# Optimization experiments

Hardware: AMD Instinct MI355X
Metric: run time of the kernel (lower is better)

The kernel has to match this reference:

```python
import jax, jax.numpy as jnp
import numpy as np

B_, N_, E_, NNZ = 64, 1723, 1723, 16384
CIN, COUT = 256, 256
H1, H2, H3 = 64, 32, 128  # lin1 out, HGCN hidden, HGCN out (hidden_channels=128)


def layernorm(x, g, b, eps=1e-5):
    mu = jnp.mean(x, axis=-1, keepdims=True)
    var = jnp.mean((x - mu) ** 2, axis=-1, keepdims=True)
    return (x - mu) * jax.lax.rsqrt(var + eps) * g + b


def graph_linear(x, W, b):
    # x: (B, Cin, N) -> (B, Cout, N), matches torch.matmul(W[None], x) + b[None,:,None]
    return jnp.einsum('oc,bcn->bon', W, x) + b[None, :, None]


def hconv(x, node_idx, edge_idx, theta, bias):
    # PyG HypergraphConv (no attention): X' = D^-1 H W B^-1 H^T X Theta + bias
    x = jnp.einsum('bnc,oc->bno', x, theta)  # lin (bias=False)
    ones = jnp.ones(node_idx.shape, x.dtype)
    Dd = jax.ops.segment_sum(ones, node_idx, num_segments=N_)  # node degree
    Bd = jax.ops.segment_sum(ones, edge_idx, num_segments=E_)  # hyperedge degree
    Dinv = jnp.where(Dd > 0, 1.0 / Dd, 0.0)
    Binv = jnp.where(Bd > 0, 1.0 / Bd, 0.0)
    # node -> hyperedge aggregation, message scaled by B^-1 of target edge
    msg = jnp.swapaxes(x[:, node_idx, :] * Binv[edge_idx][None, :, None], 0, 1)  # (nnz,B,C)
    ef = jax.ops.segment_sum(msg, edge_idx, num_segments=E_)  # (E,B,C)
    # hyperedge -> node aggregation, message scaled by D^-1 of target node
    msg2 = ef[edge_idx] * Dinv[node_idx][:, None, None]  # (nnz,B,C)
    out = jax.ops.segment_sum(msg2, node_idx, num_segments=N_)  # (N,B,C)
    return jnp.swapaxes(out, 0, 1) + bias


def setup_inputs():
    key = jax.random.key(0)
    ks = jax.random.split(key, 8)
    s = 0.02
    return {
        'x': jax.random.normal(ks[0], (B_, N_, CIN), jnp.float32),
        'incident_matrix': jax.random.randint(ks[1], (2, NNZ), 0, N_, jnp.int32),
        'pre_g': jnp.ones((CIN,), jnp.float32),
        'pre_b': jnp.zeros((CIN,), jnp.float32),
        'lin1_W': jax.random.normal(ks[2], (H1, CIN), jnp.float32) * s,
        'lin1_b': jnp.zeros((H1,), jnp.float32),
        'n1_g': jnp.ones((H1,), jnp.float32),
        'n1_b': jnp.zeros((H1,), jnp.float32),
        'th1': jax.random.normal(ks[3], (H2, H1), jnp.float32) * s,
        'bi1': jnp.zeros((H2,), jnp.float32),
        'th2': jax.random.normal(ks[4], (H3, H2), jnp.float32) * s,
        'bi2': jnp.zeros((H3,), jnp.float32),
        'n2_g': jnp.ones((H3,), jnp.float32),
        'n2_b': jnp.zeros((H3,), jnp.float32),
        'lin2_W': jax.random.normal(ks[5], (COUT, H3), jnp.float32) * s,
        'lin2_b': jnp.zeros((COUT,), jnp.float32),
    }


def reference(x, incident_matrix, pre_g, pre_b, lin1_W, lin1_b, n1_g, n1_b,
              th1, bi1, th2, bi2, n2_g, n2_b, lin2_W, lin2_b):
    node_idx, edge_idx = incident_matrix[0], incident_matrix[1]
    ty = jnp.swapaxes(jax.nn.relu(layernorm(x, pre_g, pre_b)), 1, 2)  # (B,Cin,N)
    y = jnp.swapaxes(graph_linear(ty, lin1_W, lin1_b), 1, 2)          # (B,N,64)
    y = jax.nn.relu(layernorm(y, n1_g, n1_b))
    y = hconv(y, node_idx, edge_idx, th1, bi1)                         # (B,N,32)
    y = hconv(y, node_idx, edge_idx, th2, bi2)                         # (B,N,128)
    ty = jnp.swapaxes(jax.nn.relu(layernorm(y, n2_g, n2_b)), 1, 2)
    y = jnp.swapaxes(graph_linear(ty, lin2_W, lin2_b), 1, 2)           # (B,N,256)
    return x + y  # skip_conv declared in module but unused in forward
```

## Files before the change

### kernel.cpp

```cpp
#include <hip/hip_runtime.h>
#include <cstdint>

constexpr int B  = 64;
constexpr int N  = 1723;
constexpr int E  = 1723;
constexpr int NNZ = 16384;
constexpr int ROWS = B * N;

typedef __bf16 bf16x8 __attribute__((ext_vector_type(8)));
typedef float  f32x4  __attribute__((ext_vector_type(4)));

constexpr size_t OFF_DD   = 0;
constexpr size_t OFF_BD   = OFF_DD + E;
constexpr size_t OFF_NCUR = OFF_BD + E;
constexpr size_t OFF_ECUR = OFF_NCUR + E;
constexpr size_t OFF_NOFF = OFF_ECUR + E;
constexpr size_t OFF_EOFF = OFF_NOFF + (E + 1);
constexpr size_t OFF_NVAL = OFF_EOFF + (E + 1);
constexpr size_t OFF_EVAL = OFF_NVAL + NNZ;

constexpr int WB_LIN1 = 0;
constexpr int WB_TH1  = 16384;
constexpr int WB_TH2  = 18432;
constexpr int WB_LIN2 = 22528;
constexpr int WB_TOT  = 55296;
constexpr int CVT_BLOCKS  = WB_TOT / 8 / 256;
constexpr int ZERO_INTS   = 4 * E;
constexpr int ZERO_BLOCKS = (ZERO_INTS + 255) / 256;

constexpr size_t B_WB    = 262144;
constexpr size_t B_SLOTA = 1u << 20;
constexpr size_t B_SLOTB = B_SLOTA + (30u << 20);
constexpr size_t B_SLOTC = B_SLOTB + (8u << 20);
constexpr size_t B_SLOTD = B_SLOTC + (8u << 20);

__device__ __forceinline__ ushort f2bf(float f) {
  uint32_t b = __float_as_uint(f);
  b += 0x7fffu + ((b >> 16) & 1u);
  return (ushort)(b >> 16);
}
__device__ __forceinline__ float bf2f(ushort u) {
  return __uint_as_float((uint32_t)u << 16);
}
union U16x8 { uint4 q; ushort s[8]; };

__global__ __launch_bounds__(256) void k_init(const float* __restrict__ W1, const float* __restrict__ W2,
                                              const float* __restrict__ W3, const float* __restrict__ W4,
                                              ushort* __restrict__ out, int* __restrict__ zr) {
  int bid = blockIdx.x;
  if (bid < CVT_BLOCKS) {
    int e = (bid * 256 + threadIdx.x) * 8;
    const float* src;
    int off;
    if (e < WB_TH1)      { src = W1; off = e - WB_LIN1; }
    else if (e < WB_TH2) { src = W2; off = e - WB_TH1; }
    else if (e < WB_LIN2){ src = W3; off = e - WB_TH2; }
    else                 { src = W4; off = e - WB_LIN2; }
    float4 v0 = *(const float4*)(src + off);
    float4 v1 = *(const float4*)(src + off + 4);
    U16x8 u;
    u.s[0] = f2bf(v0.x); u.s[1] = f2bf(v0.y); u.s[2] = f2bf(v0.z); u.s[3] = f2bf(v0.w);
    u.s[4] = f2bf(v1.x); u.s[5] = f2bf(v1.y); u.s[6] = f2bf(v1.z); u.s[7] = f2bf(v1.w);
    *(uint4*)(out + e) = u.q;
  } else {
    int i = (bid - CVT_BLOCKS) * 256 + threadIdx.x;
    if (i < ZERO_INTS) zr[i] = 0;
  }
}

__global__ __launch_bounds__(256) void k_hist(const int* __restrict__ inc,
                                              int* __restrict__ Dd, int* __restrict__ Bd) {
  int k = blockIdx.x * 256 + threadIdx.x;
  atomicAdd(&Dd[inc[k]], 1);
  atomicAdd(&Bd[inc[NNZ + k]], 1);
}

__global__ __launch_bounds__(256) void k_scan(const int* __restrict__ Dd, const int* __restrict__ Bd,
                                              int* __restrict__ noff, int* __restrict__ eoff) {
  __shared__ int part[256];
  const int t = threadIdx.x;
  for (int pass = 0; pass < 2; ++pass) {
    const int* cnt = pass ? Bd : Dd;
    int* off = pass ? eoff : noff;
    constexpr int CH = 7;
    int loc[CH];
    int s = 0;
    int base = t * CH;
#pragma unroll
    for (int i = 0; i < CH; ++i) {
      int idx = base + i;
      loc[i] = (idx < E) ? cnt[idx] : 0;
      s += loc[i];
    }
    part[t] = s;
    __syncthreads();
    for (int d = 1; d < 256; d <<= 1) {
      int v = (t >= d) ? part[t - d] : 0;
      __syncthreads();
      part[t] += v;
      __syncthreads();
    }
    int pre = (t > 0) ? part[t - 1] : 0;
#pragma unroll
    for (int i = 0; i < CH; ++i) {
      int idx = base + i;
      if (idx < E) off[idx] = pre;
      pre += loc[i];
    }
    if (t == 255) off[E] = pre;
    __syncthreads();
  }
}

__global__ __launch_bounds__(256) void k_fill(const int* __restrict__ inc,
                                              const int* __restrict__ noff, const int* __restrict__ eoff,
                                              int* __restrict__ ncur, int* __restrict__ ecur,
                                              int* __restrict__ nval, int* __restrict__ eval) {
  int k = blockIdx.x * 256 + threadIdx.x;
  int n = inc[k], e = inc[NNZ + k];
  int p = atomicAdd(&ecur[e], 1);
  eval[eoff[e] + p] = n;
  int q = atomicAdd(&ncur[n], 1);
  nval[noff[n] + q] = e;
}

__global__ __launch_bounds__(256) void k_sort2(const int* __restrict__ noff, int* __restrict__ nval,
                                               const int* __restrict__ eoff, int* __restrict__ eval) {
  int s = blockIdx.x * 256 + threadIdx.x;
  const int* off;
  int* vals;
  if (s < E) { off = noff; vals = nval; }
  else if (s < 2 * E) { off = eoff; vals = eval; s -= E; }
  else return;
  int b = off[s], e = off[s + 1];
  for (int i = b + 1; i < e; ++i) {
    int v = vals[i];
    int j = i - 1;
    while (j >= b && vals[j] > v) { vals[j + 1] = vals[j]; --j; }
    vals[j + 1] = v;
  }
}

__global__ __launch_bounds__(256, 3) void k_lin1th1(const float* __restrict__ x,
                                                    const ushort* __restrict__ Wb,
                                                    const float* __restrict__ lin1_b,
                                                    const float* __restrict__ pre_g,
                                                    const float* __restrict__ pre_b,
                                                    const float* __restrict__ n1_g,
                                                    const float* __restrict__ n1_b,
                                                    ushort* __restrict__ xl1) {
  __shared__ __align__(16) uint4 R0[2048];
  __shared__ __align__(16) uint4 W2s[256];
  __shared__ float2 st[64];

  const int t = threadIdx.x;
  const int r0 = blockIdx.x * 64;
  const ushort* W1 = Wb + WB_LIN1;
  const ushort* W2 = Wb + WB_TH1;

  const int lane = t & 63;
  const int w = t >> 6;
  const int lo = lane & 15, hi = lane >> 4;
  const int wm = w & 1, wn = w >> 1;
  const int m0 = wm * 32 + lo, m1 = wm * 32 + 16 + lo;

  bf16x8 wf[16];
#pragma unroll
  for (int ks = 0; ks < 8; ++ks)
#pragma unroll
    for (int f = 0; f < 2; ++f) {
      int n = wn * 32 + f * 16 + lo;
      wf[ks * 2 + f] = *(const bf16x8*)(W1 + (size_t)n * 256 + (ks * 4 + hi) * 8);
    }

  {
    int row = t >> 3, c = t & 7;
    W2s[row * 8 + (c ^ (row & 7))] = *(const uint4*)(W2 + row * 64 + c * 8);
  }
#pragma unroll
  for (int i = 0; i < 8; ++i) {
    int idx = t + i * 256;
    int row = idx >> 5, c = idx & 31;
    const float* src = x + (size_t)(r0 + row) * 256 + c * 8;
    float4 v0 = *(const float4*)src;
    float4 v1 = *(const float4*)(src + 4);
    U16x8 u;
    u.s[0] = f2bf(v0.x); u.s[1] = f2bf(v0.y); u.s[2] = f2bf(v0.z); u.s[3] = f2bf(v0.w);
    u.s[4] = f2bf(v1.x); u.s[5] = f2bf(v1.y); u.s[6] = f2bf(v1.z); u.s[7] = f2bf(v1.w);
    R0[row * 32 + (c ^ (row & 7))] = u.q;
  }
  __syncthreads();

  {
    int row = t >> 2, part = t & 3;
    float s1 = 0.f, s2 = 0.f;
#pragma unroll
    for (int i = 0; i < 8; ++i) {
      int c = part * 8 + i;
      U16x8 u; u.q = R0[row * 32 + (c ^ (row & 7))];
#pragma unroll
      for (int j = 0; j < 8; ++j) { float v = bf2f(u.s[j]); s1 += v; s2 += v * v; }
    }
    s1 += __shfl_xor(s1, 1, 64); s2 += __shfl_xor(s2, 1, 64);
    s1 += __shfl_xor(s1, 2, 64); s2 += __shfl_xor(s2, 2, 64);
    if (part == 0) {
      float mu = s1 / 256.f;
      float var = fmaxf(s2 / 256.f - mu * mu, 0.f);
      st[row] = make_float2(mu, rsqrtf(var + 1e-5f));
    }
  }
  __syncthreads();
#pragma unroll
  for (int i = 0; i < 8; ++i) {
    int idx = t + i * 256;
    int row = idx >> 5, c = idx & 31;
    int slot = row * 32 + (c ^ (row & 7));
    U16x8 u; u.q = R0[slot];
    float2 s = st[row];
    float4 g0 = *(const float4*)(pre_g + c * 8);
    float4 g1 = *(const float4*)(pre_g + c * 8 + 4);
    float4 b0 = *(const float4*)(pre_b + c * 8);
    float4 b1 = *(const float4*)(pre_b + c * 8 + 4);
    U16x8 o;
    o.s[0] = f2bf(fmaxf(fmaf((bf2f(u.s[0]) - s.x) * s.y, g0.x, b0.x), 0.f));
    o.s[1] = f2bf(fmaxf(fmaf((bf2f(u.s[1]) - s.x) * s.y, g0.y, b0.y), 0.f));
    o.s[2] = f2bf(fmaxf(fmaf((bf2f(u.s[2]) - s.x) * s.y, g0.z, b0.z), 0.f));
    o.s[3] = f2bf(fmaxf(fmaf((bf2f(u.s[3]) - s.x) * s.y, g0.w, b0.w), 0.f));
    o.s[4] = f2bf(fmaxf(fmaf((bf2f(u.s[4]) - s.x) * s.y, g1.x, b1.x), 0.f));
    o.s[5] = f2bf(fmaxf(fmaf((bf2f(u.s[5]) - s.x) * s.y, g1.y, b1.y), 0.f));
    o.s[6] = f2bf(fmaxf(fmaf((bf2f(u.s[6]) - s.x) * s.y, g1.z, b1.z), 0.f));
    o.s[7] = f2bf(fmaxf(fmaf((bf2f(u.s[7]) - s.x) * s.y, g1.w, b1.w), 0.f));
    R0[slot] = o.q;
  }
  __syncthreads();

  const bf16x8* Asv = (const bf16x8*)R0;
  f32x4 acc1[2][2] = {};
#pragma unroll
  for (int ks = 0; ks < 8; ++ks) {
    int cb = ks * 4 + hi;
    bf16x8 a0 = Asv[m0 * 32 + (cb ^ (m0 & 7))];
    bf16x8 a1 = Asv[m1 * 32 + (cb ^ (m1 & 7))];
#pragma unroll
    for (int f = 0; f < 2; ++f) {
      acc1[0][f] = __builtin_amdgcn_mfma_f32_16x16x32_bf16(a0, wf[ks * 2 + f], acc1[0][f], 0, 0, 0);
      acc1[1][f] = __builtin_amdgcn_mfma_f32_16x16x32_bf16(a1, wf[ks * 2 + f], acc1[1][f], 0, 0, 0);
    }
  }
  __syncthreads();

  float* ost = (float*)R0;
#pragma unroll
  for (int f = 0; f < 2; ++f) {
    int colg = wn * 32 + f * 16 + lo;
    float badd = lin1_b[colg];
#pragma unroll
    for (int i = 0; i < 2; ++i)
#pragma unroll
      for (int r = 0; r < 4; ++r) {
        int lr = wm * 32 + i * 16 + hi * 4 + r;
        ost[lr * 68 + colg] = acc1[i][f][r] + badd;
      }
  }
  __syncthreads();

  {
    int row = t >> 2, part = t & 3;
    float s1 = 0.f, s2 = 0.f;
#pragma unroll
    for (int i = 0; i < 16; ++i) {
      float v = ost[row * 68 + part * 16 + i];
      s1 += v; s2 += v * v;
    }
    s1 += __shfl_xor(s1, 1, 64); s2 += __shfl_xor(s2, 1, 64);
    s1 += __shfl_xor(s1, 2, 64); s2 += __shfl_xor(s2, 2, 64);
    if (part == 0) {
      float mu = s1 / 64.f;
      float var = fmaxf(s2 / 64.f - mu * mu, 0.f);
      st[row] = make_float2(mu, rsqrtf(var + 1e-5f));
    }
  }
  __syncthreads();
  uint4* A2q = R0 + 1152;
#pragma unroll
  for (int i = 0; i < 2; ++i) {
    int idx = t + i * 256;
    int row = idx >> 3, c = idx & 7;
    float2 s = st[row];
    U16x8 u;
#pragma unroll
    for (int j = 0; j < 8; ++j) {
      int col = c * 8 + j;
      float v = ost[row * 68 + col];
      u.s[j] = f2bf(fmaxf(fmaf((v - s.x) * s.y, n1_g[col], n1_b[col]), 0.f));
    }
    A2q[row * 8 + (c ^ (row & 7))] = u.q;
  }
  __syncthreads();

  const bf16x8* A2v = (const bf16x8*)A2q;
  f32x4 acc2[2] = {};
#pragma unroll
  for (int ks = 0; ks < 2; ++ks) {
    int cb = ks * 4 + hi;
    bf16x8 a0 = A2v[m0 * 8 + (cb ^ (m0 & 7))];
    bf16x8 a1 = A2v[m1 * 8 + (cb ^ (m1 & 7))];
    int n = wn * 16 + lo;
    bf16x8 bfr = ((const bf16x8*)W2s)[n * 8 + (cb ^ (n & 7))];
    acc2[0] = __builtin_amdgcn_mfma_f32_16x16x32_bf16(a0, bfr, acc2[0], 0, 0, 0);
    acc2[1] = __builtin_amdgcn_mfma_f32_16x16x32_bf16(a1, bfr, acc2[1], 0, 0, 0);
  }
  {
    int colg = wn * 16 + lo;
#pragma unroll
    for (int i = 0; i < 2; ++i)
#pragma unroll
      for (int r = 0; r < 4; ++r) {
        int lr = wm * 32 + i * 16 + hi * 4 + r;
        ost[lr * 36 + colg] = acc2[i][r];
      }
  }
  __syncthreads();
  {
    int lr = t >> 2, c8 = t & 3;
    uint32_t r = r0 + lr;
    uint32_t b_ = r / (uint32_t)N;
    uint32_t n_ = r - b_ * (uint32_t)N;
    U16x8 u;
#pragma unroll
    for (int j = 0; j < 8; ++j) u.s[j] = f2bf(ost[lr * 36 + c8 * 8 + j]);
    *(uint4*)(xl1 + ((size_t)n_ * 64 + b_) * 32 + c8 * 8) = u.q;
  }
}

template <bool HASB>
__global__ __launch_bounds__(256) void agg_bf16_k(const ushort* __restrict__ in,
                                                  const int* __restrict__ off,
                                                  const int* __restrict__ vals,
                                                  const float* __restrict__ bias,
                                                  ushort* __restrict__ outb) {
  const int seg = blockIdx.x;
  const int beg = off[seg], end = off[seg + 1];
  const int t = threadIdx.x;
  float acc[8] = {0.f, 0.f, 0.f, 0.f, 0.f, 0.f, 0.f, 0.f};
  for (int k = beg; k < end; ++k) {
    int src = vals[k];
    U16x8 u;
    u.q = *(const uint4*)(in + (size_t)src * 2048 + t * 8);
#pragma unroll
    for (int j = 0; j < 8; ++j) acc[j] += bf2f(u.s[j]);
  }
  float inv = (end > beg) ? 1.f / (float)(end - beg) : 0.f;
  U16x8 o;
  if constexpr (HASB) {
    int cb = (t & 3) * 8;
#pragma unroll
    for (int j = 0; j < 8; ++j) o.s[j] = f2bf(acc[j] * inv + bias[cb + j]);
  } else {
#pragma unroll
    for (int j = 0; j < 8; ++j) o.s[j] = f2bf(acc[j] * inv);
  }
  *(uint4*)(outb + (size_t)seg * 2048 + t * 8) = o.q;
}

__global__ __launch_bounds__(256, 2) void k_aggth2(const ushort* __restrict__ ef2,
                                                   const int* __restrict__ noff,
                                                   const int* __restrict__ nval,
                                                   const ushort* __restrict__ W2b,
                                                   const float* __restrict__ bi2,
                                                   const float* __restrict__ n2_g,
                                                   const float* __restrict__ n2_b,
                                                   ushort* __restrict__ y3n) {
  __shared__ __align__(16) uint4 A2s[256];
  __shared__ __align__(16) uint4 W2s[512];
  __shared__ float ost[64 * 132];
  __shared__ float2 st[64];
  const int t = threadIdx.x;
  const int seg = blockIdx.x;

#pragma unroll
  for (int i = 0; i < 2; ++i) {
    int idx = t + i * 256;
    int row = idx >> 2, c = idx & 3;
    W2s[row * 4 + (c ^ (row & 3))] = *(const uint4*)(W2b + row * 32 + c * 8);
  }
  const int beg = noff[seg], end = noff[seg + 1];
  float acc[8] = {0.f, 0.f, 0.f, 0.f, 0.f, 0.f, 0.f, 0.f};
  for (int k = beg; k < end; ++k) {
    int src = nval[k];
    U16x8 u;
    u.q = *(const uint4*)(ef2 + (size_t)src * 2048 + t * 8);
#pragma unroll
    for (int j = 0; j < 8; ++j) acc[j] += bf2f(u.s[j]);
  }
  float inv = (end > beg) ? 1.f / (float)(end - beg) : 0.f;
  {
    U16x8 u;
#pragma unroll
    for (int j = 0; j < 8; ++j) u.s[j] = f2bf(acc[j] * inv);
    int row = t >> 2, c = t & 3;
    A2s[row * 4 + (c ^ (row & 3))] = u.q;
  }
  __syncthreads();

  const int lane = t & 63;
  const int w = t >> 6;
  const int lo = lane & 15, hi = lane >> 4;
  const int wm = w & 1, wn = w >> 1;
  const int m0 = wm * 32 + lo, m1 = wm * 32 + 16 + lo;
  const bf16x8* Asv = (const bf16x8*)A2s;
  const bf16x8* Wsv = (const bf16x8*)W2s;
  f32x4 acc2[2][4] = {};
  {
    bf16x8 a0 = Asv[m0 * 4 + (hi ^ (m0 & 3))];
    bf16x8 a1 = Asv[m1 * 4 + (hi ^ (m1 & 3))];
#pragma unroll
    for (int f = 0; f < 4; ++f) {
      int n = wn * 64 + f * 16 + lo;
      bf16x8 bfr = Wsv[n * 4 + (hi ^ (n & 3))];
      acc2[0][f] = __builtin_amdgcn_mfma_f32_16x16x32_bf16(a0, bfr, acc2[0][f], 0, 0, 0);
      acc2[1][f] = __builtin_amdgcn_mfma_f32_16x16x32_bf16(a1, bfr, acc2[1][f], 0, 0, 0);
    }
  }
#pragma unroll
  for (int f = 0; f < 4; ++f) {
    int colg = wn * 64 + f * 16 + lo;
    float badd = bi2[colg];
#pragma unroll
    for (int i = 0; i < 2; ++i)
#pragma unroll
      for (int r = 0; r < 4; ++r) {
        int lr = wm * 32 + i * 16 + hi * 4 + r;
        ost[lr * 132 + colg] = acc2[i][f][r] + badd;
      }
  }
  __syncthreads();
  {
    int row = t >> 2, part = t & 3;
    float s1 = 0.f, s2 = 0.f;
#pragma unroll
    for (int i = 0; i < 32; ++i) {
      float v = ost[row * 132 + part * 32 + i];
      s1 += v; s2 += v * v;
    }
    s1 += __shfl_xor(s1, 1, 64); s2 += __shfl_xor(s2, 1, 64);
    s1 += __shfl_xor(s1, 2, 64); s2 += __shfl_xor(s2, 2, 64);
    if (part == 0) {
      float mu = s1 / 128.f;
      float var = fmaxf(s2 / 128.f - mu * mu, 0.f);
      st[row] = make_float2(mu, rsqrtf(var + 1e-5f));
    }
  }
  __syncthreads();
#pragma unroll
  for (int i = 0; i < 4; ++i) {
    int idx = t + i * 256;
    int row = idx >> 4, c = idx & 15;
    float2 s = st[row];
    U16x8 u;
#pragma unroll
    for (int j = 0; j < 8; ++j) {
      int col = c * 8 + j;
      float v = ost[row * 132 + col];
      u.s[j] = f2bf(fmaxf(fmaf((v - s.x) * s.y, n2_g[col], n2_b[col]), 0.f));
    }
    *(uint4*)(y3n + ((size_t)seg * 64 + row) * 128 + c * 8) = u.q;
  }
}

constexpr int NWG2 = (ROWS / 64) * 4;
__global__ __launch_bounds__(256, 2) void k_lin2(const ushort* __restrict__ y3n,
                                                 const ushort* __restrict__ Wl2,
                                                 const float* __restrict__ lin2_b,
                                                 const float* __restrict__ x,
                                                 float* __restrict__ out) {
  __shared__ __align__(16) uint4 smem[2048];
  const int t = threadIdx.x;
  int orig = blockIdx.x;
  int xcd = orig & 7;
  int idx0 = orig >> 3;
  constexpr int q = NWG2 / 8, r = NWG2 % 8;
  int wgid = (xcd < r ? xcd * (q + 1) : r * (q + 1) + (xcd - r) * q) + idx0;
  const int tile = wgid & 3;
  const int r0 = (wgid >> 2) * 64;
  const int c0 = tile * 64;
  uint4* AsQ = smem;
  uint4* WsQ = smem + 1024;

#pragma unroll
  for (int i = 0; i < 4; ++i) {
    int idx = t + i * 256;
    int row = idx >> 4, c = idx & 15;
    AsQ[row * 16 + (c ^ (row & 7))] = *(const uint4*)(y3n + (size_t)(r0 + row) * 128 + c * 8);
  }
#pragma unroll
  for (int i = 0; i < 4; ++i) {
    int idx = t + i * 256;
    int row = idx >> 4, c = idx & 15;
    WsQ[row * 16 + (c ^ (row & 7))] = *(const uint4*)(Wl2 + (size_t)(c0 + row) * 128 + c * 8);
  }
  __syncthreads();

  const int lane = t & 63;
  const int w = t >> 6;
  const int lo = lane & 15, hi = lane >> 4;
  const int wm = w & 1, wn = w >> 1;
  const int m0 = wm * 32 + lo, m1 = wm * 32 + 16 + lo;
  const bf16x8* Asv = (const bf16x8*)AsQ;
  const bf16x8* Wsv = (const bf16x8*)WsQ;
  f32x4 acc[2][2] = {};
#pragma unroll
  for (int ks = 0; ks < 4; ++ks) {
    int cb = ks * 4 + hi;
    bf16x8 a0 = Asv[m0 * 16 + (cb ^ (m0 & 7))];
    bf16x8 a1 = Asv[m1 * 16 + (cb ^ (m1 & 7))];
#pragma unroll
    for (int f = 0; f < 2; ++f) {
      int n = wn * 32 + f * 16 + lo;
      bf16x8 bfr = Wsv[n * 16 + (cb ^ (n & 7))];
      acc[0][f] = __builtin_amdgcn_mfma_f32_16x16x32_bf16(a0, bfr, acc[0][f], 0, 0, 0);
      acc[1][f] = __builtin_amdgcn_mfma_f32_16x16x32_bf16(a1, bfr, acc[1][f], 0, 0, 0);
    }
  }
  __syncthreads();

  float* ost = (float*)smem;
#pragma unroll
  for (int f = 0; f < 2; ++f) {
    int cl = wn * 32 + f * 16 + lo;
    float badd = lin2_b[c0 + cl];
#pragma unroll
    for (int i = 0; i < 2; ++i)
#pragma unroll
      for (int r2 = 0; r2 < 4; ++r2) {
        int lr = wm * 32 + i * 16 + hi * 4 + r2;
        ost[lr * 68 + cl] = acc[i][f][r2] + badd;
      }
  }
  __syncthreads();

#pragma unroll
  for (int i = 0; i < 4; ++i) {
    int idx = t + i * 256;
    int lr = idx >> 4, c4 = idx & 15;
    uint32_t rr = r0 + lr;
    uint32_t n_ = rr >> 6, b_ = rr & 63u;
    size_t obase = ((size_t)b_ * N + n_) * 256 + c0 + c4 * 4;
    float4 v = *(const float4*)&ost[lr * 68 + c4 * 4];
    float4 s = *(const float4*)(x + obase);
    v.x += s.x; v.y += s.y; v.z += s.z; v.w += s.w;
    *(float4*)(out + obase) = v;
  }
}

extern "C" void kernel_launch(void* const* d_in, const int* in_sizes, int n_in,
                              void* d_out, int out_size, void* d_ws, size_t ws_size,
                              hipStream_t stream) {
  const float* x      = (const float*)d_in[0];
  const int*   inc    = (const int*)  d_in[1];
  const float* pre_g  = (const float*)d_in[2];
  const float* pre_b  = (const float*)d_in[3];
  const float* lin1_W = (const float*)d_in[4];
  const float* lin1_b = (const float*)d_in[5];
  const float* n1_g   = (const float*)d_in[6];
  const float* n1_b   = (const float*)d_in[7];
  const float* th1    = (const float*)d_in[8];
  const float* bi1    = (const float*)d_in[9];
  const float* th2    = (const float*)d_in[10];
  const float* bi2    = (const float*)d_in[11];
  const float* n2_g   = (const float*)d_in[12];
  const float* n2_b   = (const float*)d_in[13];
  const float* lin2_W = (const float*)d_in[14];
  const float* lin2_b = (const float*)d_in[15];
  float* out = (float*)d_out;
  char* ws = (char*)d_ws;

  int* meta = (int*)ws;
  int* Dd   = meta + OFF_DD;
  int* Bd   = meta + OFF_BD;
  int* ncur = meta + OFF_NCUR;
  int* ecur = meta + OFF_ECUR;
  int* noff = meta + OFF_NOFF;
  int* eoff = meta + OFF_EOFF;
  int* nval = meta + OFF_NVAL;
  int* eval = meta + OFF_EVAL;

  ushort* Wbase = (ushort*)(ws + B_WB);
  ushort* y3n = (ushort*)(ws + B_SLOTA);
  ushort* xl1 = (ushort*)(ws + B_SLOTB);
  ushort* ef2 = (ushort*)(ws + B_SLOTB);
  ushort* ef1 = (ushort*)(ws + B_SLOTC);
  ushort* y2  = (ushort*)(ws + B_SLOTD);

  k_init<<<CVT_BLOCKS + ZERO_BLOCKS, 256, 0, stream>>>(lin1_W, th1, th2, lin2_W, Wbase, meta);

  k_hist<<<NNZ / 256, 256, 0, stream>>>(inc, Dd, Bd);
  k_scan<<<1, 256, 0, stream>>>(Dd, Bd, noff, eoff);
  k_fill<<<NNZ / 256, 256, 0, stream>>>(inc, noff, eoff, ncur, ecur, nval, eval);
  k_sort2<<<(2 * E + 255) / 256, 256, 0, stream>>>(noff, nval, eoff, eval);

  k_lin1th1<<<ROWS / 64, 256, 0, stream>>>(x, Wbase, lin1_b, pre_g, pre_b, n1_g, n1_b, xl1);

  agg_bf16_k<false><<<E, 256, 0, stream>>>(xl1, eoff, eval, nullptr, ef1);
  agg_bf16_k<true ><<<E, 256, 0, stream>>>(ef1, noff, nval, bi1, y2);
  agg_bf16_k<false><<<E, 256, 0, stream>>>(y2, eoff, eval, nullptr, ef2);

  k_aggth2<<<E, 256, 0, stream>>>(ef2, noff, nval, Wbase + WB_TH2, bi2, n2_g, n2_b, y3n);

  k_lin2<<<NWG2, 256, 0, stream>>>(y3n, Wbase + WB_LIN2, lin2_b, x, out);
}
```

Baseline: 182.7 us.

## Fuse CSR build into one cooperative kernel and prefetch gathers in aggregation

Replaces five small preprocessing launches (weight conversion/zeroing, histogram, scan, fill, sort) with one cooperative kernel of 64 blocks that uses grid-wide syncs between phases. The cursors are initialised from the offsets so the fill writes directly. The aggregation loops also software-prefetch the next gathered row before accumulating the current one. This aims to cut launch overhead and gather latency, at the cost of grid.sync barriers and a cooperative launch.

```diff
diff --git a/kernel.cpp b/kernel.cpp
--- a/kernel.cpp
+++ b/kernel.cpp
@@ -1,5 +1,8 @@
 #include <hip/hip_runtime.h>
+#include <hip/hip_cooperative_groups.h>
 #include <cstdint>
+
+namespace cg = cooperative_groups;
 
 constexpr int B  = 64;
 constexpr int N  = 1723;
@@ -24,9 +27,6 @@
 constexpr int WB_TH2  = 18432;
 constexpr int WB_LIN2 = 22528;
 constexpr int WB_TOT  = 55296;
-constexpr int CVT_BLOCKS  = WB_TOT / 8 / 256;
-constexpr int ZERO_INTS   = 4 * E;
-constexpr int ZERO_BLOCKS = (ZERO_INTS + 255) / 256;
 
 constexpr size_t B_WB    = 262144;
 constexpr size_t B_SLOTA = 1u << 20;
@@ -44,12 +44,23 @@
 }
 union U16x8 { uint4 q; ushort s[8]; };
 
-__global__ __launch_bounds__(256) void k_init(const float* __restrict__ W1, const float* __restrict__ W2,
-                                              const float* __restrict__ W3, const float* __restrict__ W4,
-                                              ushort* __restrict__ out, int* __restrict__ zr) {
-  int bid = blockIdx.x;
-  if (bid < CVT_BLOCKS) {
-    int e = (bid * 256 + threadIdx.x) * 8;
+__global__ __launch_bounds__(256) void k_csr(const int* __restrict__ inc,
+                                             const float* __restrict__ W1, const float* __restrict__ W2,
+                                             const float* __restrict__ W3, const float* __restrict__ W4,
+                                             ushort* __restrict__ wout,
+                                             int* __restrict__ cntN, int* __restrict__ cntE,
+                                             int* __restrict__ noff, int* __restrict__ eoff,
+                                             int* __restrict__ ncur, int* __restrict__ ecur,
+                                             int* __restrict__ nval, int* __restrict__ eval) {
+  cg::grid_group grid = cg::this_grid();
+  const int t = threadIdx.x;
+  const int tid = blockIdx.x * 256 + t;
+  __shared__ int part[256];
+
+  if (tid < E) cntN[tid] = 0;
+  else if (tid < 2 * E) cntE[tid - E] = 0;
+  if (tid < WB_TOT / 8) {
+    int e = tid * 8;
     const float* src;
     int off;
     if (e < WB_TH1)      { src = W1; off = e - WB_LIN1; }
@@ -61,83 +72,72 @@
     U16x8 u;
     u.s[0] = f2bf(v0.x); u.s[1] = f2bf(v0.y); u.s[2] = f2bf(v0.z); u.s[3] = f2bf(v0.w);
     u.s[4] = f2bf(v1.x); u.s[5] = f2bf(v1.y); u.s[6] = f2bf(v1.z); u.s[7] = f2bf(v1.w);
-    *(uint4*)(out + e) = u.q;
-  } else {
-    int i = (bid - CVT_BLOCKS) * 256 + threadIdx.x;
-    if (i < ZERO_INTS) zr[i] = 0;
-  }
-}
-
-__global__ __launch_bounds__(256) void k_hist(const int* __restrict__ inc,
-                                              int* __restrict__ Dd, int* __restrict__ Bd) {
-  int k = blockIdx.x * 256 + threadIdx.x;
-  atomicAdd(&Dd[inc[k]], 1);
-  atomicAdd(&Bd[inc[NNZ + k]], 1);
-}
-
-__global__ __launch_bounds__(256) void k_scan(const int* __restrict__ Dd, const int* __restrict__ Bd,
-                                              int* __restrict__ noff, int* __restrict__ eoff) {
-  __shared__ int part[256];
-  const int t = threadIdx.x;
-  for (int pass = 0; pass < 2; ++pass) {
-    const int* cnt = pass ? Bd : Dd;
-    int* off = pass ? eoff : noff;
-    constexpr int CH = 7;
-    int loc[CH];
-    int s = 0;
-    int base = t * CH;
-#pragma unroll
-    for (int i = 0; i < CH; ++i) {
-      int idx = base + i;
-      loc[i] = (idx < E) ? cnt[idx] : 0;
-      s += loc[i];
-    }
-    part[t] = s;
-    __syncthreads();
-    for (int d = 1; d < 256; d <<= 1) {
-      int v = (t >= d) ? part[t - d] : 0;
+    *(uint4*)(wout + e) = u.q;
+  }
+  grid.sync();
+
+  atomicAdd(&cntN[inc[tid]], 1);
+  atomicAdd(&cntE[inc[NNZ + tid]], 1);
+  grid.sync();
+
+  if (blockIdx.x == 0) {
+    for (int pass = 0; pass < 2; ++pass) {
+      const int* cnt = pass ? cntE : cntN;
+      int* off = pass ? eoff : noff;
+      int* cur = pass ? ecur : ncur;
+      constexpr int CH = 7;
+      int loc[CH];
+      int s = 0;
+      int base = t * CH;
+#pragma unroll
+      for (int i = 0; i < CH; ++i) {
+        int idx = base + i;
+        loc[i] = (idx < E) ? cnt[idx] : 0;
+        s += loc[i];
+      }
+      part[t] = s;
       __syncthreads();
-      part[t] += v;
+      for (int d = 1; d < 256; d <<= 1) {
+        int v = (t >= d) ? part[t - d] : 0;
+        __syncthreads();
+        part[t] += v;
+        __syncthreads();
+      }
+      int pre = (t > 0) ? part[t - 1] : 0;
+#pragma unroll
+      for (int i = 0; i < CH; ++i) {
+        int idx = base + i;
+        if (idx < E) { off[idx] = pre; cur[idx] = pre; }
+        pre += loc[i];
+      }
+      if (t == 255) off[E] = pre;
       __syncthreads();
     }
-    int pre = (t > 0) ? part[t - 1] : 0;
-#pragma unroll
-    for (int i = 0; i < CH; ++i) {
-      int idx = base + i;
-      if (idx < E) off[idx] = pre;
-      pre += loc[i];
-    }
-    if (t == 255) off[E] = pre;
-    __syncthreads();
-  }
-}
-
-__global__ __launch_bounds__(256) void k_fill(const int* __restrict__ inc,
-                                              const int* __restrict__ noff, const int* __restrict__ eoff,
-                                              int* __restrict__ ncur, int* __restrict__ ecur,
-                                              int* __restrict__ nval, int* __restrict__ eval) {
-  int k = blockIdx.x * 256 + threadIdx.x;
-  int n = inc[k], e = inc[NNZ + k];
-  int p = atomicAdd(&ecur[e], 1);
-  eval[eoff[e] + p] = n;
-  int q = atomicAdd(&ncur[n], 1);
-  nval[noff[n] + q] = e;
-}
-
-__global__ __launch_bounds__(256) void k_sort2(const int* __restrict__ noff, int* __restrict__ nval,
-                                               const int* __restrict__ eoff, int* __restrict__ eval) {
-  int s = blockIdx.x * 256 + threadIdx.x;
-  const int* off;
-  int* vals;
-  if (s < E) { off = noff; vals = nval; }
-  else if (s < 2 * E) { off = eoff; vals = eval; s -= E; }
-  else return;
-  int b = off[s], e = off[s + 1];
-  for (int i = b + 1; i < e; ++i) {
-    int v = vals[i];
-    int j = i - 1;
-    while (j >= b && vals[j] > v) { vals[j + 1] = vals[j]; --j; }
-    vals[j + 1] = v;
+  }
+  grid.sync();
+
+  {
+    int n = inc[tid], e = inc[NNZ + tid];
+    int p = atomicAdd(&ecur[e], 1);
+    eval[p] = n;
+    int q = atomicAdd(&ncur[n], 1);
+    nval[q] = e;
+  }
+  grid.sync();
+
+  if (tid < 2 * E) {
+    int s = tid;
+    const int* off;
+    int* vals;
+    if (s < E) { off = noff; vals = nval; }
+    else { off = eoff; vals = eval; s -= E; }
+    int b = off[s], e2 = off[s + 1];
+    for (int i = b + 1; i < e2; ++i) {
+      int v = vals[i];
+      int j = i - 1;
+      while (j >= b && vals[j] > v) { vals[j + 1] = vals[j]; --j; }
+      vals[j + 1] = v;
+    }
   }
 }
 
@@ -343,10 +343,16 @@
   const int beg = off[seg], end = off[seg + 1];
   const int t = threadIdx.x;
   float acc[8] = {0.f, 0.f, 0.f, 0.f, 0.f, 0.f, 0.f, 0.f};
-  for (int k = beg; k < end; ++k) {
-    int src = vals[k];
-    U16x8 u;
-    u.q = *(const uint4*)(in + (size_t)src * 2048 + t * 8);
+  if (beg < end) {
+    uint4 cur = *(const uint4*)(in + (size_t)vals[beg] * 2048 + t * 8);
+    for (int k = beg + 1; k < end; ++k) {
+      uint4 nxt = *(const uint4*)(in + (size_t)vals[k] * 2048 + t * 8);
+      U16x8 u; u.q = cur;
+#pragma unroll
+      for (int j = 0; j < 8; ++j) acc[j] += bf2f(u.s[j]);
+      cur = nxt;
+    }
+    U16x8 u; u.q = cur;
 #pragma unroll
     for (int j = 0; j < 8; ++j) acc[j] += bf2f(u.s[j]);
   }
@@ -386,10 +392,16 @@
   }
   const int beg = noff[seg], end = noff[seg + 1];
   float acc[8] = {0.f, 0.f, 0.f, 0.f, 0.f, 0.f, 0.f, 0.f};
-  for (int k = beg; k < end; ++k) {
-    int src = nval[k];
-    U16x8 u;
-    u.q = *(const uint4*)(ef2 + (size_t)src * 2048 + t * 8);
+  if (beg < end) {
+    uint4 cur = *(const uint4*)(ef2 + (size_t)nval[beg] * 2048 + t * 8);
+    for (int k = beg + 1; k < end; ++k) {
+      uint4 nxt = *(const uint4*)(ef2 + (size_t)nval[k] * 2048 + t * 8);
+      U16x8 u; u.q = cur;
+#pragma unroll
+      for (int j = 0; j < 8; ++j) acc[j] += bf2f(u.s[j]);
+      cur = nxt;
+    }
+    U16x8 u; u.q = cur;
 #pragma unroll
     for (int j = 0; j < 8; ++j) acc[j] += bf2f(u.s[j]);
   }
@@ -576,8 +588,8 @@
   char* ws = (char*)d_ws;
 
   int* meta = (int*)ws;
-  int* Dd   = meta + OFF_DD;
-  int* Bd   = meta + OFF_BD;
+  int* cntN = meta + OFF_DD;
+  int* cntE = meta + OFF_BD;
   int* ncur = meta + OFF_NCUR;
   int* ecur = meta + OFF_ECUR;
   int* noff = meta + OFF_NOFF;
@@ -592,12 +604,12 @@
   ushort* ef1 = (ushort*)(ws + B_SLOTC);
   ushort* y2  = (ushort*)(ws + B_SLOTD);
 
-  k_init<<<CVT_BLOCKS + ZERO_BLOCKS, 256, 0, stream>>>(lin1_W, th1, th2, lin2_W, Wbase, meta);
-
-  k_hist<<<NNZ / 256, 256, 0, stream>>>(inc, Dd, Bd);
-  k_scan<<<1, 256, 0, stream>>>(Dd, Bd, noff, eoff);
-  k_fill<<<NNZ / 256, 256, 0, stream>>>(inc, noff, eoff, ncur, ecur, nval, eval);
-  k_sort2<<<(2 * E + 255) / 256, 256, 0, stream>>>(noff, nval, eoff, eval);
+  {
+    void* args[] = {(void*)&inc, (void*)&lin1_W, (void*)&th1, (void*)&th2, (void*)&lin2_W,
+                    (void*)&Wbase, (void*)&cntN, (void*)&cntE, (void*)&noff, (void*)&eoff,
+                    (void*)&ncur, (void*)&ecur, (void*)&nval, (void*)&eval};
+    hipLaunchCooperativeKernel((void*)k_csr, dim3(64), dim3(256), args, 0, stream);
+  }
 
   k_lin1th1<<<ROWS / 64, 256, 0, stream>>>(x, Wbase, lin1_b, pre_g, pre_b, n1_g, n1_b, xl1);
 
```

Measured after the change: 222.9 us. 22.0% more time.
